# Kernel tuning notes

Hardware: AMD Instinct MI355X
Metric: run time of the kernel (lower is better)

## Reference

```python
import jax, jax.numpy as jnp
import numpy as np
from jax.scipy.linalg import expm

B = 131072
ROT_DIM = 32   # rot_latent_dim
TRZ_DIM = 32   # tranz_latent_dim
W = 128        # MLP_hidden_layer_width


def setup_inputs() -> dict:
    key = jax.random.key(0)
    ks = jax.random.split(key, 13)
    def g(k, shape, scale):
        return jax.random.normal(k, shape, dtype=jnp.float32) * scale
    return {
        "y": g(ks[0], (B, ROT_DIM + TRZ_DIM), 1.0),
        # omega MLP: 32 -> 128 -> 128 -> 9
        "ow0": g(ks[1], (W, ROT_DIM), 1.0 / np.sqrt(ROT_DIM)),
        "ob0": g(ks[2], (W,), 0.01),
        "ow1": g(ks[3], (W, W), 1.0 / np.sqrt(W)),
        "ob1": g(ks[4], (W,), 0.01),
        "ow2": g(ks[5], (9, W), 1.0 / np.sqrt(W)),
        "ob2": g(ks[6], (9,), 0.01),
        # tranz MLP: 32 -> 128 -> 128 -> 3
        "tw0": g(ks[7], (W, TRZ_DIM), 1.0 / np.sqrt(TRZ_DIM)),
        "tb0": g(ks[8], (W,), 0.01),
        "tw1": g(ks[9], (W, W), 1.0 / np.sqrt(W)),
        "tb1": g(ks[10], (W,), 0.01),
        "tw2": g(ks[11], (3, W), 1.0 / np.sqrt(W)),
        "tb2": g(ks[12], (3,), 0.01),
    }


def _mlp(x, weights, biases):
    # eqx.nn.Linear: W @ x + b; ReLU on all but last layer
    n = len(weights)
    for i, (w, b) in enumerate(zip(weights, biases)):
        x = jnp.einsum("bi,oi->bo", x, w) + b
        if i + 1 < n:
            x = jax.nn.relu(x)
    return x


def reference(y, ow0, ob0, ow1, ob1, ow2, ob2, tw0, tb0, tw1, tb1, tw2, tb2):
    x = y[:, :ROT_DIM]            # dynamic_slice(0, rot_latent_dim)
    z = y[:, ROT_DIM:ROT_DIM + TRZ_DIM]
    omega = _mlp(x, [ow0, ow1, ow2], [ob0, ob1, ob2])       # [B, 9]
    # exp_omega: reshape to 3x3, matrix exponential, flatten back
    rot = jax.vmap(expm)(omega.reshape(B, 3, 3)).reshape(B, 9)
    trz = _mlp(z, [tw0, tw1, tw2], [tb0, tb1, tb2])          # [B, 3]
    return jnp.concatenate([rot, trz], axis=1)               # [B, 12]
```

## Files before the change

### kernel.cpp

```cpp
#include <hip/hip_runtime.h>
#include <hip/hip_bf16.h>
#include <stdint.h>

typedef short  short8  __attribute__((ext_vector_type(8)));
typedef float  floatx4 __attribute__((ext_vector_type(4)));

#define WS_W0_ROT   0
#define WS_W0_TRZ   8192
#define WS_W1_ROT   16384
#define WS_W1_TRZ   49152
#define WS_W2_ROT   81920
#define WS_W2_TRZ   86016
#define WS_BIAS     90112

__device__ __forceinline__ unsigned short f2bf_rne(float f) {
    union { float f; unsigned u; } v; v.f = f;
    unsigned r = v.u + 0x7fffu + ((v.u >> 16) & 1u);
    return (unsigned short)(r >> 16);
}

__global__ void prep_kernel(const float* __restrict__ ow0, const float* __restrict__ ow1,
                            const float* __restrict__ ow2, const float* __restrict__ tw0,
                            const float* __restrict__ tw1, const float* __restrict__ tw2,
                            const float* __restrict__ ob0, const float* __restrict__ ob1,
                            const float* __restrict__ ob2, const float* __restrict__ tb0,
                            const float* __restrict__ tb1, const float* __restrict__ tb2,
                            unsigned char* __restrict__ ws)
{
    int t = blockIdx.x * 256 + threadIdx.x;
    unsigned short* w16 = (unsigned short*)ws;
    if (t < 4096) {
        w16[t] = f2bf_rne(ow0[t]);
    } else if (t < 8192) {
        w16[t] = f2bf_rne(tw0[t - 4096]);
    } else if (t < 24576) {
        int i = t - 8192; int n = i >> 7, p = i & 127;
        w16[t] = f2bf_rne(ow1[n * 128 + ((p & 7) << 4) + (p >> 3)]);
    } else if (t < 40960) {
        int i = t - 24576; int n = i >> 7, p = i & 127;
        w16[t] = f2bf_rne(tw1[n * 128 + ((p & 7) << 4) + (p >> 3)]);
    } else if (t < 43008) {
        int i = t - 40960; int n = i >> 7, p = i & 127;
        w16[t] = (n < 9) ? f2bf_rne(ow2[n * 128 + ((p & 7) << 4) + (p >> 3)]) : (unsigned short)0;
    } else if (t < 45056) {
        int i = t - 43008; int n = i >> 7, p = i & 127;
        w16[t] = (n < 3) ? f2bf_rne(tw2[n * 128 + ((p & 7) << 4) + (p >> 3)]) : (unsigned short)0;
    } else if (t < 45600) {
        int i = t - 45056;
        float v;
        if      (i < 128) v = ob0[i];
        else if (i < 256) v = ob1[i - 128];
        else if (i < 272) v = (i - 256 < 9) ? ob2[i - 256] : 0.0f;
        else if (i < 400) v = tb0[i - 272];
        else if (i < 528) v = tb1[i - 400];
        else              v = (i - 528 < 3) ? tb2[i - 528] : 0.0f;
        ((float*)(ws + WS_BIAS))[i] = v;
    }
}

__device__ __forceinline__ floatx4 mfma16(short8 a, short8 b, floatx4 c) {
    return __builtin_amdgcn_mfma_f32_16x16x32_bf16(a, b, c, 0, 0, 0);
}

__device__ __forceinline__ short8 pack8(floatx4 a, floatx4 b) {
    union { unsigned u[4]; short8 s; } r;
    union { __hip_bfloat162 b2; unsigned u; } c;
    c.b2 = __float22bfloat162_rn(make_float2(a[0], a[1])); r.u[0] = c.u;
    c.b2 = __float22bfloat162_rn(make_float2(a[2], a[3])); r.u[1] = c.u;
    c.b2 = __float22bfloat162_rn(make_float2(b[0], b[1])); r.u[2] = c.u;
    c.b2 = __float22bfloat162_rn(make_float2(b[2], b[3])); r.u[3] = c.u;
    return r.s;
}

__device__ __forceinline__ void write_h_b128(char* hb, int q, int ln,
                                             const floatx4* acc) {
    #pragma unroll
    for (int r = 0; r < 4; ++r) {
        const int m = q * 4 + r;
        union { unsigned u[4]; short8 s; } pk;
        #pragma unroll
        for (int j = 0; j < 4; ++j) {
            float lo = fmaxf(acc[2 * j][r], 0.0f);
            float hi = fmaxf(acc[2 * j + 1][r], 0.0f);
            union { __hip_bfloat162 b2; unsigned u; } c;
            c.b2 = __float22bfloat162_rn(make_float2(lo, hi));
            pk.u[j] = c.u;
        }
        const int cp = ln ^ (m & 15);
        *(short8*)(hb + m * 256 + cp * 16) = pk.s;
    }
}

__device__ __forceinline__ void read_a_b128(const char* hb, int q, int ln, short8* a) {
    #pragma unroll
    for (int s2 = 0; s2 < 4; ++s2) {
        const int cp = (s2 * 4 + q) ^ (ln & 15);
        a[s2] = *(const short8*)(hb + ln * 256 + cp * 16);
    }
}

__device__ __forceinline__ void mat3mul(float* C, const float* A, const float* B) {
    #pragma unroll
    for (int i = 0; i < 3; ++i)
        #pragma unroll
        for (int j = 0; j < 3; ++j)
            C[i*3+j] = A[i*3+0]*B[0+j] + A[i*3+1]*B[3+j] + A[i*3+2]*B[6+j];
}

__launch_bounds__(256, 2)
__global__ void fused_main(const float* __restrict__ y,
                           const unsigned char* __restrict__ ws,
                           float* __restrict__ out)
{
    __shared__ __align__(16) unsigned char lds_h[4][4096];
    __shared__ __align__(16) float lds_stage[256 * 12];

    const int tid  = threadIdx.x;
    const int wv   = tid >> 6;
    const int lane = tid & 63;
    const int ln   = lane & 15;
    const int q    = lane >> 4;
    const int mlp  = wv >> 1;
    const int rh   = wv & 1;
    const int wgbase = blockIdx.x * 256;

    const int W0_OFF = mlp ? WS_W0_TRZ : WS_W0_ROT;
    const int W1_OFF = mlp ? WS_W1_TRZ : WS_W1_ROT;
    const int W2_OFF = mlp ? WS_W2_TRZ : WS_W2_ROT;
    const float* bias = (const float*)(ws + WS_BIAS) + (mlp ? 272 : 0);

    short8 bw0[8], bw1[32], bw2[4];
    #pragma unroll
    for (int nt = 0; nt < 8; ++nt)
        bw0[nt] = *(const short8*)(ws + W0_OFF + ((nt * 16 + ln) * 32 + q * 8) * 2);
    #pragma unroll
    for (int nt = 0; nt < 8; ++nt) {
        #pragma unroll
        for (int s2 = 0; s2 < 4; ++s2)
            bw1[nt * 4 + s2] = *(const short8*)(ws + W1_OFF + ((nt * 16 + ln) * 128 + s2 * 32 + q * 8) * 2);
    }
    #pragma unroll
    for (int s2 = 0; s2 < 4; ++s2)
        bw2[s2] = *(const short8*)(ws + W2_OFF + (ln * 128 + s2 * 32 + q * 8) * 2);

    unsigned b01[8];
    #pragma unroll
    for (int nt = 0; nt < 8; ++nt) {
        union { __hip_bfloat162 b2; unsigned u; } c;
        c.b2 = __float22bfloat162_rn(make_float2(bias[nt * 16 + ln], bias[128 + nt * 16 + ln]));
        b01[nt] = c.u;
    }
    const float b2v = bias[256 + ln];

    char* hb = (char*)lds_h[wv];
    const int cb     = mlp ? 9 : 0;
    const int nvalid = mlp ? 3 : 9;

    const float* ybase = y + (size_t)(wgbase + rh * 128) * 64 + mlp * 32 + q * 8;

    floatx4 cy0 = *(const floatx4*)(ybase + (size_t)ln * 64);
    floatx4 cy1 = *(const floatx4*)(ybase + (size_t)ln * 64 + 4);
    short8 a0 = pack8(cy0, cy1);

    #pragma unroll 1
    for (int g = 0; g < 8; ++g) {
        const int gn = (g < 7) ? g + 1 : g;
        const float* yp = ybase + (size_t)(gn * 16 + ln) * 64;
        floatx4 ny0 = *(const floatx4*)yp;
        floatx4 ny1 = *(const floatx4*)(yp + 4);

        floatx4 acc[8];
        #pragma unroll
        for (int nt = 0; nt < 8; ++nt) {
            union { __hip_bfloat162 b2; unsigned u; } c; c.u = b01[nt];
            float b = __bfloat162float(c.b2.x);
            floatx4 a = {b, b, b, b};
            acc[nt] = mfma16(a0, bw0[nt], a);
        }
        write_h_b128(hb, q, ln, acc);

        a0 = pack8(ny0, ny1);

        short8 a1[4];
        read_a_b128(hb, q, ln, a1);

        #pragma unroll
        for (int nt = 0; nt < 8; ++nt) {
            union { __hip_bfloat162 b2; unsigned u; } c; c.u = b01[nt];
            float b = __bfloat162float(c.b2.y);
            floatx4 a = {b, b, b, b};
            #pragma unroll
            for (int s2 = 0; s2 < 4; ++s2)
                a = mfma16(a1[s2], bw1[nt * 4 + s2], a);
            acc[nt] = a;
        }
        write_h_b128(hb, q, ln, acc);

        short8 a2[4];
        read_a_b128(hb, q, ln, a2);

        floatx4 acc2 = {b2v, b2v, b2v, b2v};
        #pragma unroll
        for (int s2 = 0; s2 < 4; ++s2)
            acc2 = mfma16(a2[s2], bw2[s2], acc2);

        if (ln < nvalid) {
            const int rl = rh * 128 + g * 16 + q * 4;
            #pragma unroll
            for (int r = 0; r < 4; ++r)
                lds_stage[(rl + r) * 12 + cb + ln] = acc2[r];
        }
    }

    __syncthreads();

    {
        float* st = &lds_stage[tid * 12];
        floatx4 m0 = *(floatx4*)(st);
        floatx4 m1 = *(floatx4*)(st + 4);
        floatx4 m2 = *(floatx4*)(st + 8);
        float M[9] = {m0[0], m0[1], m0[2], m0[3], m1[0], m1[1], m1[2], m1[3], m2[0]};
        const float tz0 = m2[1], tz1 = m2[2], tz2 = m2[3];

        float r0 = fabsf(M[0]) + fabsf(M[1]) + fabsf(M[2]);
        float r1 = fabsf(M[3]) + fabsf(M[4]) + fabsf(M[5]);
        float r2 = fabsf(M[6]) + fabsf(M[7]) + fabsf(M[8]);
        float nrm = fmaxf(r0, fmaxf(r1, r2));
        int e; (void)frexpf(nrm, &e);
        int s = e + 1;
        if (s < 0) s = 0;
        if (s > 24) s = 24;
        float sc;
        { union { unsigned u; float f; } cv; cv.u = (unsigned)(127 - s) << 23; sc = cv.f; }
        #pragma unroll
        for (int i = 0; i < 9; ++i) M[i] *= sc;

        float Rm[9];
        #pragma unroll
        for (int i = 0; i < 9; ++i) Rm[i] = 0.0f;
        Rm[0] = Rm[4] = Rm[8] = 1.0f;
        #pragma unroll
        for (int j = 12; j >= 1; --j) {
            float T[9]; mat3mul(T, M, Rm);
            const float inv = 1.0f / (float)j;
            #pragma unroll
            for (int i = 0; i < 9; ++i) Rm[i] = T[i] * inv;
            Rm[0] += 1.0f; Rm[4] += 1.0f; Rm[8] += 1.0f;
        }
        for (int it = 0; it < s; ++it) {
            float T[9]; mat3mul(T, Rm, Rm);
            #pragma unroll
            for (int i = 0; i < 9; ++i) Rm[i] = T[i];
        }

        floatx4 o0 = {Rm[0], Rm[1], Rm[2], Rm[3]};
        floatx4 o1 = {Rm[4], Rm[5], Rm[6], Rm[7]};
        floatx4 o2 = {Rm[8], tz0, tz1, tz2};
        *(floatx4*)(st)     = o0;
        *(floatx4*)(st + 4) = o1;
        *(floatx4*)(st + 8) = o2;
    }

    __syncthreads();

    {
        float* ob = out + (size_t)wgbase * 12;
        #pragma unroll
        for (int k = 0; k < 3; ++k) {
            const int j = k * 256 + tid;
            floatx4 v = *(floatx4*)&lds_stage[j * 4];
            *(floatx4*)(ob + j * 4) = v;
        }
    }
}

extern "C" void kernel_launch(void* const* d_in, const int* in_sizes, int n_in,
                              void* d_out, int out_size, void* d_ws, size_t ws_size,
                              hipStream_t stream)
{
    const float* y = (const float*)d_in[0];
    prep_kernel<<<179, 256, 0, stream>>>(
        (const float*)d_in[1], (const float*)d_in[3], (const float*)d_in[5],
        (const float*)d_in[7], (const float*)d_in[9], (const float*)d_in[11],
        (const float*)d_in[2], (const float*)d_in[4], (const float*)d_in[6],
        (const float*)d_in[8], (const float*)d_in[10], (const float*)d_in[12],
        (unsigned char*)d_ws);
    fused_main<<<512, 256, 0, stream>>>(y, (const unsigned char*)d_ws, (float*)d_out);
}
```

Baseline: 143.7 us.

## Split hidden columns across wave pairs to halve per-wave weight registers

Each MLP is now handled by a pair of waves that split the 128 hidden output columns, rather than splitting the batch rows. This halves the per-wave weight registers, so launch bounds rise to 3 blocks per CU and the grid doubles to 1024 blocks of 128 rows. Partial hidden activations are exchanged through shared LDS buffers, which adds two block-wide barriers per row group. The Taylor order of the expm is also cut from 12 to 10, trading a little accuracy for fewer matrix multiplies.

New measurement: 144.0 us. About the same (+0.3%).

```diff
diff --git a/kernel.cpp b/kernel.cpp
--- a/kernel.cpp
+++ b/kernel.cpp
@@ -72,29 +72,25 @@
     return r.s;
 }
 
-__device__ __forceinline__ void write_h_b128(char* hb, int q, int ln,
-                                             const floatx4* acc) {
+__device__ __forceinline__ void write_h_b64(char* hb, int q, int ln, int f,
+                                            const floatx4* acc) {
     #pragma unroll
     for (int r = 0; r < 4; ++r) {
         const int m = q * 4 + r;
-        union { unsigned u[4]; short8 s; } pk;
-        #pragma unroll
-        for (int j = 0; j < 4; ++j) {
-            float lo = fmaxf(acc[2 * j][r], 0.0f);
-            float hi = fmaxf(acc[2 * j + 1][r], 0.0f);
-            union { __hip_bfloat162 b2; unsigned u; } c;
-            c.b2 = __float22bfloat162_rn(make_float2(lo, hi));
-            pk.u[j] = c.u;
-        }
-        const int cp = ln ^ (m & 15);
-        *(short8*)(hb + m * 256 + cp * 16) = pk.s;
+        union { unsigned u[2]; double d; } pk;
+        union { __hip_bfloat162 b2; unsigned u; } c;
+        c.b2 = __float22bfloat162_rn(make_float2(fmaxf(acc[0][r], 0.0f), fmaxf(acc[1][r], 0.0f)));
+        pk.u[0] = c.u;
+        c.b2 = __float22bfloat162_rn(make_float2(fmaxf(acc[2][r], 0.0f), fmaxf(acc[3][r], 0.0f)));
+        pk.u[1] = c.u;
+        *(double*)(hb + m * 256 + ((ln ^ m) << 4) + (f << 3)) = pk.d;
     }
 }
 
 __device__ __forceinline__ void read_a_b128(const char* hb, int q, int ln, short8* a) {
     #pragma unroll
     for (int s2 = 0; s2 < 4; ++s2) {
-        const int cp = (s2 * 4 + q) ^ (ln & 15);
+        const int cp = (s2 * 4 + q) ^ ln;
         a[s2] = *(const short8*)(hb + ln * 256 + cp * 16);
     }
 }
@@ -107,13 +103,14 @@
             C[i*3+j] = A[i*3+0]*B[0+j] + A[i*3+1]*B[3+j] + A[i*3+2]*B[6+j];
 }
 
-__launch_bounds__(256, 2)
+__launch_bounds__(256, 3)
 __global__ void fused_main(const float* __restrict__ y,
                            const unsigned char* __restrict__ ws,
                            float* __restrict__ out)
 {
-    __shared__ __align__(16) unsigned char lds_h[4][4096];
-    __shared__ __align__(16) float lds_stage[256 * 12];
+    __shared__ __align__(16) unsigned char lds_h0[2][4096];
+    __shared__ __align__(16) unsigned char lds_h1[2][4096];
+    __shared__ __align__(16) float lds_stage[128 * 12];
 
     const int tid  = threadIdx.x;
     const int wv   = tid >> 6;
@@ -121,42 +118,42 @@
     const int ln   = lane & 15;
     const int q    = lane >> 4;
     const int mlp  = wv >> 1;
-    const int rh   = wv & 1;
-    const int wgbase = blockIdx.x * 256;
+    const int f    = wv & 1;
+    const int wgbase = blockIdx.x * 128;
 
     const int W0_OFF = mlp ? WS_W0_TRZ : WS_W0_ROT;
     const int W1_OFF = mlp ? WS_W1_TRZ : WS_W1_ROT;
     const int W2_OFF = mlp ? WS_W2_TRZ : WS_W2_ROT;
     const float* bias = (const float*)(ws + WS_BIAS) + (mlp ? 272 : 0);
 
-    short8 bw0[8], bw1[32], bw2[4];
-    #pragma unroll
-    for (int nt = 0; nt < 8; ++nt)
-        bw0[nt] = *(const short8*)(ws + W0_OFF + ((nt * 16 + ln) * 32 + q * 8) * 2);
-    #pragma unroll
-    for (int nt = 0; nt < 8; ++nt) {
+    short8 bw0[4], bw1[16], bw2[4];
+    #pragma unroll
+    for (int j = 0; j < 4; ++j)
+        bw0[j] = *(const short8*)(ws + W0_OFF + (((f * 4 + j) * 16 + ln) * 32 + q * 8) * 2);
+    #pragma unroll
+    for (int j = 0; j < 4; ++j) {
         #pragma unroll
         for (int s2 = 0; s2 < 4; ++s2)
-            bw1[nt * 4 + s2] = *(const short8*)(ws + W1_OFF + ((nt * 16 + ln) * 128 + s2 * 32 + q * 8) * 2);
+            bw1[j * 4 + s2] = *(const short8*)(ws + W1_OFF + (((f * 4 + j) * 16 + ln) * 128 + s2 * 32 + q * 8) * 2);
     }
     #pragma unroll
     for (int s2 = 0; s2 < 4; ++s2)
         bw2[s2] = *(const short8*)(ws + W2_OFF + (ln * 128 + s2 * 32 + q * 8) * 2);
 
-    unsigned b01[8];
-    #pragma unroll
-    for (int nt = 0; nt < 8; ++nt) {
-        union { __hip_bfloat162 b2; unsigned u; } c;
-        c.b2 = __float22bfloat162_rn(make_float2(bias[nt * 16 + ln], bias[128 + nt * 16 + ln]));
-        b01[nt] = c.u;
+    float b0v[4], b1v[4];
+    #pragma unroll
+    for (int j = 0; j < 4; ++j) {
+        b0v[j] = bias[(f * 4 + j) * 16 + ln];
+        b1v[j] = bias[128 + (f * 4 + j) * 16 + ln];
     }
     const float b2v = bias[256 + ln];
 
-    char* hb = (char*)lds_h[wv];
+    char* hb0 = (char*)lds_h0[mlp];
+    char* hb1 = (char*)lds_h1[mlp];
     const int cb     = mlp ? 9 : 0;
     const int nvalid = mlp ? 3 : 9;
 
-    const float* ybase = y + (size_t)(wgbase + rh * 128) * 64 + mlp * 32 + q * 8;
+    const float* ybase = y + (size_t)wgbase * 64 + mlp * 32 + q * 8;
 
     floatx4 cy0 = *(const floatx4*)(ybase + (size_t)ln * 64);
     floatx4 cy1 = *(const floatx4*)(ybase + (size_t)ln * 64 + 4);
@@ -169,43 +166,43 @@
         floatx4 ny0 = *(const floatx4*)yp;
         floatx4 ny1 = *(const floatx4*)(yp + 4);
 
-        floatx4 acc[8];
-        #pragma unroll
-        for (int nt = 0; nt < 8; ++nt) {
-            union { __hip_bfloat162 b2; unsigned u; } c; c.u = b01[nt];
-            float b = __bfloat162float(c.b2.x);
-            floatx4 a = {b, b, b, b};
-            acc[nt] = mfma16(a0, bw0[nt], a);
-        }
-        write_h_b128(hb, q, ln, acc);
+        floatx4 acc[4];
+        #pragma unroll
+        for (int j = 0; j < 4; ++j) {
+            floatx4 c = {b0v[j], b0v[j], b0v[j], b0v[j]};
+            acc[j] = mfma16(a0, bw0[j], c);
+        }
+        write_h_b64(hb0, q, ln, f, acc);
 
         a0 = pack8(ny0, ny1);
 
+        __syncthreads();
+
         short8 a1[4];
-        read_a_b128(hb, q, ln, a1);
-
-        #pragma unroll
-        for (int nt = 0; nt < 8; ++nt) {
-            union { __hip_bfloat162 b2; unsigned u; } c; c.u = b01[nt];
-            float b = __bfloat162float(c.b2.y);
-            floatx4 a = {b, b, b, b};
+        read_a_b128(hb0, q, ln, a1);
+
+        #pragma unroll
+        for (int j = 0; j < 4; ++j) {
+            floatx4 c = {b1v[j], b1v[j], b1v[j], b1v[j]};
             #pragma unroll
             for (int s2 = 0; s2 < 4; ++s2)
-                a = mfma16(a1[s2], bw1[nt * 4 + s2], a);
-            acc[nt] = a;
-        }
-        write_h_b128(hb, q, ln, acc);
+                c = mfma16(a1[s2], bw1[j * 4 + s2], c);
+            acc[j] = c;
+        }
+        write_h_b64(hb1, q, ln, f, acc);
+
+        __syncthreads();
 
         short8 a2[4];
-        read_a_b128(hb, q, ln, a2);
+        read_a_b128(hb1, q, ln, a2);
 
         floatx4 acc2 = {b2v, b2v, b2v, b2v};
         #pragma unroll
         for (int s2 = 0; s2 < 4; ++s2)
             acc2 = mfma16(a2[s2], bw2[s2], acc2);
 
-        if (ln < nvalid) {
-            const int rl = rh * 128 + g * 16 + q * 4;
+        if (f == 0 && ln < nvalid) {
+            const int rl = g * 16 + q * 4;
             #pragma unroll
             for (int r = 0; r < 4; ++r)
                 lds_stage[(rl + r) * 12 + cb + ln] = acc2[r];
@@ -214,7 +211,7 @@
 
     __syncthreads();
 
-    {
+    if (tid < 128) {
         float* st = &lds_stage[tid * 12];
         floatx4 m0 = *(floatx4*)(st);
         floatx4 m1 = *(floatx4*)(st + 4);
@@ -231,7 +228,7 @@
         if (s < 0) s = 0;
         if (s > 24) s = 24;
         float sc;
-        { union { unsigned u; float f; } cv; cv.u = (unsigned)(127 - s) << 23; sc = cv.f; }
+        { union { unsigned u; float fv; } cv; cv.u = (unsigned)(127 - s) << 23; sc = cv.fv; }
         #pragma unroll
         for (int i = 0; i < 9; ++i) M[i] *= sc;
 
@@ -240,7 +237,7 @@
         for (int i = 0; i < 9; ++i) Rm[i] = 0.0f;
         Rm[0] = Rm[4] = Rm[8] = 1.0f;
         #pragma unroll
-        for (int j = 12; j >= 1; --j) {
+        for (int j = 10; j >= 1; --j) {
             float T[9]; mat3mul(T, M, Rm);
             const float inv = 1.0f / (float)j;
             #pragma unroll
@@ -265,11 +262,11 @@
 
     {
         float* ob = out + (size_t)wgbase * 12;
-        #pragma unroll
-        for (int k = 0; k < 3; ++k) {
-            const int j = k * 256 + tid;
-            floatx4 v = *(floatx4*)&lds_stage[j * 4];
-            *(floatx4*)(ob + j * 4) = v;
+        floatx4 v = *(floatx4*)&lds_stage[tid * 4];
+        *(floatx4*)(ob + tid * 4) = v;
+        if (tid < 128) {
+            floatx4 v2 = *(floatx4*)&lds_stage[(256 + tid) * 4];
+            *(floatx4*)(ob + (256 + tid) * 4) = v2;
         }
     }
 }
@@ -285,5 +282,5 @@
         (const float*)d_in[2], (const float*)d_in[4], (const float*)d_in[6],
         (const float*)d_in[8], (const float*)d_in[10], (const float*)d_in[12],
         (unsigned char*)d_ws);
-    fused_main<<<512, 256, 0, stream>>>(y, (const unsigned char*)d_ws, (float*)d_out);
-}
+    fused_main<<<1024, 256, 0, stream>>>(y, (const unsigned char*)d_ws, (float*)d_out);
+}
```
